# Performance work log

Measured on AMD Instinct MI355X. Metric: run time of the kernel, lower is better.

## Reference

```python
import jax, jax.numpy as jnp
import numpy as np

B, P, L1, D = 64, 16, 16, 1024  # images, people/img, object slots/img (slot0=no-object), feat dim
SP = 32   # flattened spatial (Conv_spatial output channels)
PROJ = 512
ACT = 29


def setup_inputs() -> dict:
    key = jax.random.key(0)
    ks = jax.random.split(key, 16)
    rn = lambda k, s, sc=1.0: jax.random.normal(k, s, dtype=jnp.float32) * sc
    w = 0.02  # weight init scale
    return {
        "people": rn(ks[0], (B, P, D)),
        "objects": rn(ks[1], (B, L1, D)),
        "context": rn(ks[2], (B, D)),
        "spatial": rn(ks[3], (B, P * L1, SP)),
        "Wvis_w": rn(ks[4], (3 * D, PROJ), w), "Wvis_b": jnp.zeros((PROJ,), jnp.float32),
        "Wspat_w": rn(ks[5], (SP, PROJ), w), "Wspat_b": jnp.zeros((PROJ,), jnp.float32),
        "Wip_w": rn(ks[6], (PROJ, 1), w), "Wip_b": jnp.zeros((1,), jnp.float32),
        "Wref_w": rn(ks[7], (PROJ, ACT), w), "Wref_b": jnp.zeros((ACT,), jnp.float32),
        "Watt_w": rn(ks[8], (PROJ, ACT), w), "Watt_b": jnp.zeros((ACT,), jnp.float32),
        "Woh_w": rn(ks[9], (D, D), w), "Woh_b": jnp.zeros((D,), jnp.float32),
        "Who_w": rn(ks[10], (D, D), w), "Who_b": jnp.zeros((D,), jnp.float32),
        "Wg_w": rn(ks[11], (2 * D, ACT), w), "Wg_b": jnp.zeros((ACT,), jnp.float32),
    }


def reference(people, objects, context, spatial,
              Wvis_w, Wvis_b, Wspat_w, Wspat_b, Wip_w, Wip_b,
              Wref_w, Wref_b, Watt_w, Watt_b,
              Woh_w, Woh_b, Who_w, Who_b, Wg_w, Wg_b):
    Bn, Pn, Dn = people.shape
    L = objects.shape[1]
    C = Bn * Pn * L

    # --- ROI.pairing: all (person, object-slot) pairs + image context -> [C, 3D]
    pe = jnp.broadcast_to(people[:, :, None, :], (Bn, Pn, L, Dn))
    ob = jnp.broadcast_to(objects[:, None, :, :], (Bn, Pn, L, Dn))
    cx = jnp.broadcast_to(context[:, None, None, :], (Bn, Pn, L, Dn))
    pairs = jnp.concatenate([pe, ob, cx], axis=-1).reshape(C, 3 * Dn)

    # --- attention / visual projection heads
    a_ho = jax.nn.relu(spatial.reshape(C, -1) @ Wspat_w + Wspat_b)   # W_Spat
    f_vis = jax.nn.relu(pairs @ Wvis_w + Wvis_b)                     # W_vis
    f_ref = f_vis * a_ho
    i_ho = f_ref @ Wip_w + Wip_b                                     # [C,1]
    interaction_prob = jax.nn.sigmoid(i_ho)
    p_ref = f_ref @ Wref_w + Wref_b                                  # [C,29]
    p_att = a_ho @ Watt_w + Watt_b                                   # [C,29]

    # --- graph message passing: adjacency = interaction probs, skipping slot 0 (no-object)
    adj = interaction_prob.reshape(Bn, Pn, L)[:, :, 1:]              # [B,P,O]
    oh = jax.nn.relu(objects[:, 1:] @ Woh_w + Woh_b)                 # W_oh on objects
    ho = jax.nn.relu(people @ Who_w + Who_b)                         # W_ho on people
    people_r = people + jnp.einsum('bpo,bod->bpd', adj, oh)
    objects_r = objects[:, 1:] + jnp.einsum('bpo,bpd->bod', adj, ho)
    objects_full = jnp.concatenate([objects[:, :1], objects_r], axis=1)  # re-attach no-object slot

    # --- refined all-pairs concat -> W_graph
    pe_r = jnp.broadcast_to(people_r[:, :, None, :], (Bn, Pn, L, Dn))
    ob_r = jnp.broadcast_to(objects_full[:, None, :, :], (Bn, Pn, L, Dn))
    pairs_g = jnp.concatenate([pe_r, ob_r], axis=-1).reshape(C, 2 * Dn)
    p_graph = pairs_g @ Wg_w + Wg_b                                  # [C,29]

    return (i_ho, p_ref, p_att, p_graph)
```

## Files before the change

### kernel.cpp

```cpp
#include <hip/hip_runtime.h>


typedef unsigned short u16;
typedef short s16x8 __attribute__((ext_vector_type(8)));
typedef float f32x4 __attribute__((ext_vector_type(4)));

__device__ __forceinline__ u16 f2b(float f) {
    union { float f; unsigned int i; } v; v.f = f;
    unsigned int r = (v.i + 0x7fffu + ((v.i >> 16) & 1u)) >> 16;
    return (u16)r;
}
__device__ __forceinline__ float b2f(u16 u) {
    union { float f; unsigned int i; } v; v.i = ((unsigned int)u) << 16; return v.f;
}
__device__ __forceinline__ unsigned int pack2(float x, float y) {
    return (unsigned int)f2b(x) | ((unsigned int)f2b(y) << 16);
}

#define OFF_WSPATT 0u
#define OFF_WREFT  32768u
#define OFF_WATTT  65536u
#define OFF_WGT    98304u
#define OFF_PP     229376u
#define OFF_PO     1277952u
#define OFF_PC     2326528u
#define OFF_ADJ    2392064u
#define OFF_HP     2457600u
#define OFF_HOF    2588672u
#define OFF_YH     2719744u
#define OFF_ZO     2850816u
#define ZERO_OFF   2457600u
#define ZERO_LEN   516096u
#define OFF_WVIST2 2973696u
#define OFF_WHOT2  6119424u
#define OFF_WOHT2  8216576u
#define OFF_PEOB   10313728u
#define OFF_OBJB   12410880u
#define OFF_CTXB   14508032u
#define OFF_SPATB  14639104u

__global__ __launch_bounds__(256) void prep_all(
    const float* __restrict__ people, const float* __restrict__ objects,
    const float* __restrict__ context, const float* __restrict__ spatial,
    const float* __restrict__ Wvis, const float* __restrict__ Who,
    const float* __restrict__ Woh, const float* __restrict__ Wspat,
    const float* __restrict__ Wref, const float* __restrict__ Watt,
    const float* __restrict__ Wg,
    u16* __restrict__ peoB, u16* __restrict__ objB, u16* __restrict__ ctxB,
    u16* __restrict__ spatB, u16* __restrict__ WvisT, u16* __restrict__ WhoT,
    u16* __restrict__ WohT, u16* __restrict__ WspatT, u16* __restrict__ WrefT,
    u16* __restrict__ WattT, u16* __restrict__ WgT)
{
    __shared__ float S[64][65];
    int bid = blockIdx.x, t = threadIdx.x;
    if (bid < 896) {
        const float* src; u16* dst; int N, K, kt, nt;
        int tb = bid;
        if (tb < 256)      { src = Who;  dst = WhoT;  K = 1024; N = 1024; kt = tb >> 4; nt = tb & 15; }
        else if (tb < 512) { tb -= 256; src = Woh;  dst = WohT;  K = 1024; N = 1024; kt = tb >> 4; nt = tb & 15; }
        else               { tb -= 512; src = Wvis; dst = WvisT; K = 3072; N = 512;  kt = tb >> 3; nt = tb & 7; }
        int k0 = kt * 64, n0 = nt * 64;
        int tx = t & 63, ty = t >> 6;
#pragma unroll
        for (int i = 0; i < 16; i++)
            S[ty + 4 * i][tx] = src[(size_t)(k0 + ty + 4 * i) * N + n0 + tx];
        __syncthreads();
#pragma unroll
        for (int i = 0; i < 16; i++)
            dst[(size_t)(n0 + ty + 4 * i) * K + k0 + tx] = f2b(S[tx][ty + 4 * i]);
        return;
    }
    int g = (bid - 896) * 256 + t;
    const int gsz = 512 * 256;
    for (int i = g; i < 524288; i += gsz) {
        float2 v = ((const float2*)people)[i];
        ((unsigned int*)peoB)[i] = pack2(v.x, v.y);
    }
    for (int i = g; i < 524288; i += gsz) {
        float2 v = ((const float2*)objects)[i];
        ((unsigned int*)objB)[i] = pack2(v.x, v.y);
    }
    for (int i = g; i < 32768; i += gsz) {
        float2 v = ((const float2*)context)[i];
        ((unsigned int*)ctxB)[i] = pack2(v.x, v.y);
    }
    for (int i = g; i < 262144; i += gsz) {
        float2 v = ((const float2*)spatial)[i];
        ((unsigned int*)spatB)[i] = pack2(v.x, v.y);
    }
    for (int i = g; i < 512 * 32; i += gsz) {
        int n = i >> 5, k = i & 31;
        WspatT[i] = f2b(Wspat[k * 512 + n]);
    }
    for (int i = g; i < 32 * 512; i += gsz) {
        int n = i >> 9, k = i & 511;
        WrefT[i] = (n < 29) ? f2b(Wref[k * 29 + n]) : (u16)0;
        WattT[i] = (n < 29) ? f2b(Watt[k * 29 + n]) : (u16)0;
    }
    for (int i = g; i < 32 * 2048; i += gsz) {
        int n = i >> 11, k = i & 2047;
        WgT[i] = (n < 29) ? f2b(Wg[k * 29 + n]) : (u16)0;
    }
}

__global__ __launch_bounds__(256) void fused_gemms(
    const u16* __restrict__ peoB, const u16* __restrict__ objB,
    const u16* __restrict__ ctxB, const u16* __restrict__ WvisT,
    const u16* __restrict__ WhoT, const float* __restrict__ Who_b,
    const u16* __restrict__ WohT, const float* __restrict__ Woh_b,
    const u16* __restrict__ WgT,
    u16* __restrict__ Pp, u16* __restrict__ Po, u16* __restrict__ Pc,
    float* __restrict__ Yh, float* __restrict__ Zo,
    float* __restrict__ Hp, float* __restrict__ HoF)
{
    __shared__ u16 T[64][72];
    int bid = blockIdx.x;
    int t = threadIdx.x;
    int lane = t & 63, w = t >> 6;
    int l16 = lane & 15, q = lane >> 4;
    int wy = w >> 1, wx = w & 1;

    if (bid < 264) {
        int bx = bid & 7, ty = bid >> 3;
        const u16* A; u16* outB; int koff, bm;
        if (ty < 16)      { A = peoB; outB = Pp; koff = 0;    bm = ty * 64; }
        else if (ty < 32) { A = objB; outB = Po; koff = 1024; bm = (ty - 16) * 64; }
        else              { A = ctxB; outB = Pc; koff = 2048; bm = 0; }
        int bn = bx * 64;

        const u16* ap0 = A + (size_t)(bm + wy * 32 + l16) * 1024 + q * 8;
        const u16* ap1 = ap0 + (size_t)16 * 1024;
        const u16* bp0 = WvisT + (size_t)(bn + wx * 32 + l16) * 3072 + koff + q * 8;
        const u16* bp1 = bp0 + (size_t)16 * 3072;

        f32x4 acc00 = {0,0,0,0}, acc01 = {0,0,0,0}, acc10 = {0,0,0,0}, acc11 = {0,0,0,0};
        s16x8 ca0 = *(const s16x8*)ap0,        ca1 = *(const s16x8*)ap1;
        s16x8 cb0 = *(const s16x8*)bp0,        cb1 = *(const s16x8*)bp1;
        s16x8 na0 = *(const s16x8*)(ap0 + 32), na1 = *(const s16x8*)(ap1 + 32);
        s16x8 nb0 = *(const s16x8*)(bp0 + 32), nb1 = *(const s16x8*)(bp1 + 32);
        ap0 += 64; ap1 += 64; bp0 += 64; bp1 += 64;
        for (int it = 0; it < 30; it++) {
            s16x8 ta0 = *(const s16x8*)ap0, ta1 = *(const s16x8*)ap1;
            s16x8 tb0 = *(const s16x8*)bp0, tb1 = *(const s16x8*)bp1;
            ap0 += 32; ap1 += 32; bp0 += 32; bp1 += 32;
            acc00 = __builtin_amdgcn_mfma_f32_16x16x32_bf16(ca0, cb0, acc00, 0, 0, 0);
            acc01 = __builtin_amdgcn_mfma_f32_16x16x32_bf16(ca0, cb1, acc01, 0, 0, 0);
            acc10 = __builtin_amdgcn_mfma_f32_16x16x32_bf16(ca1, cb0, acc10, 0, 0, 0);
            acc11 = __builtin_amdgcn_mfma_f32_16x16x32_bf16(ca1, cb1, acc11, 0, 0, 0);
            ca0 = na0; ca1 = na1; cb0 = nb0; cb1 = nb1;
            na0 = ta0; na1 = ta1; nb0 = tb0; nb1 = tb1;
        }
        acc00 = __builtin_amdgcn_mfma_f32_16x16x32_bf16(ca0, cb0, acc00, 0, 0, 0);
        acc01 = __builtin_amdgcn_mfma_f32_16x16x32_bf16(ca0, cb1, acc01, 0, 0, 0);
        acc10 = __builtin_amdgcn_mfma_f32_16x16x32_bf16(ca1, cb0, acc10, 0, 0, 0);
        acc11 = __builtin_amdgcn_mfma_f32_16x16x32_bf16(ca1, cb1, acc11, 0, 0, 0);
        acc00 = __builtin_amdgcn_mfma_f32_16x16x32_bf16(na0, nb0, acc00, 0, 0, 0);
        acc01 = __builtin_amdgcn_mfma_f32_16x16x32_bf16(na0, nb1, acc01, 0, 0, 0);
        acc10 = __builtin_amdgcn_mfma_f32_16x16x32_bf16(na1, nb0, acc10, 0, 0, 0);
        acc11 = __builtin_amdgcn_mfma_f32_16x16x32_bf16(na1, nb1, acc11, 0, 0, 0);

        f32x4 accs[2][2] = {{acc00, acc01}, {acc10, acc11}};
#pragma unroll
        for (int ii = 0; ii < 2; ii++)
#pragma unroll
            for (int jj = 0; jj < 2; jj++) {
                int col = bn + wx * 32 + jj * 16 + l16;
#pragma unroll
                for (int r = 0; r < 4; r++) {
                    int row = bm + wy * 32 + ii * 16 + q * 4 + r;
                    outB[(size_t)row * 512 + col] = f2b(accs[ii][jj][r]);
                }
            }
    } else if (bid < 760) {
        int r3 = bid - 264;
        int z, rt, nbt;
        if (r3 < 256) { z = 0; rt = r3 >> 4; nbt = r3 & 15; }
        else          { z = 1; r3 -= 256; rt = r3 >> 4; nbt = r3 & 15; }
        const u16* A    = z ? objB : peoB;
        const u16* W1T  = z ? WohT : WhoT;
        const float* bb = z ? Woh_b : Who_b;
        const u16* Wg2  = z ? WgT : WgT + 1024;
        float* U        = z ? Zo : Yh;
        int m0 = rt * 64, nb = nbt * 64;

        int r0 = m0 + wy * 32 + l16;
        int r1 = r0 + 16;
        if (z) { r0 = (r0 / 15) * 16 + (r0 % 15) + 1;
                 r1 = (r1 / 15) * 16 + (r1 % 15) + 1; }
        const u16* ap0 = A + (size_t)r0 * 1024 + q * 8;
        const u16* ap1 = A + (size_t)r1 * 1024 + q * 8;
        const u16* bp0 = W1T + (size_t)(nb + wx * 32 + l16) * 1024 + q * 8;
        const u16* bp1 = bp0 + (size_t)16 * 1024;

        f32x4 acc00 = {0,0,0,0}, acc01 = {0,0,0,0}, acc10 = {0,0,0,0}, acc11 = {0,0,0,0};
        s16x8 ca0 = *(const s16x8*)ap0,        ca1 = *(const s16x8*)ap1;
        s16x8 cb0 = *(const s16x8*)bp0,        cb1 = *(const s16x8*)bp1;
        s16x8 na0 = *(const s16x8*)(ap0 + 32), na1 = *(const s16x8*)(ap1 + 32);
        s16x8 nb0 = *(const s16x8*)(bp0 + 32), nb1 = *(const s16x8*)(bp1 + 32);
        ap0 += 64; ap1 += 64; bp0 += 64; bp1 += 64;
        for (int it = 0; it < 30; it++) {
            s16x8 ta0 = *(const s16x8*)ap0, ta1 = *(const s16x8*)ap1;
            s16x8 tb0 = *(const s16x8*)bp0, tb1 = *(const s16x8*)bp1;
            ap0 += 32; ap1 += 32; bp0 += 32; bp1 += 32;
            acc00 = __builtin_amdgcn_mfma_f32_16x16x32_bf16(ca0, cb0, acc00, 0, 0, 0);
            acc01 = __builtin_amdgcn_mfma_f32_16x16x32_bf16(ca0, cb1, acc01, 0, 0, 0);
            acc10 = __builtin_amdgcn_mfma_f32_16x16x32_bf16(ca1, cb0, acc10, 0, 0, 0);
            acc11 = __builtin_amdgcn_mfma_f32_16x16x32_bf16(ca1, cb1, acc11, 0, 0, 0);
            ca0 = na0; ca1 = na1; cb0 = nb0; cb1 = nb1;
            na0 = ta0; na1 = ta1; nb0 = tb0; nb1 = tb1;
        }
        acc00 = __builtin_amdgcn_mfma_f32_16x16x32_bf16(ca0, cb0, acc00, 0, 0, 0);
        acc01 = __builtin_amdgcn_mfma_f32_16x16x32_bf16(ca0, cb1, acc01, 0, 0, 0);
        acc10 = __builtin_amdgcn_mfma_f32_16x16x32_bf16(ca1, cb0, acc10, 0, 0, 0);
        acc11 = __builtin_amdgcn_mfma_f32_16x16x32_bf16(ca1, cb1, acc11, 0, 0, 0);
        acc00 = __builtin_amdgcn_mfma_f32_16x16x32_bf16(na0, nb0, acc00, 0, 0, 0);
        acc01 = __builtin_amdgcn_mfma_f32_16x16x32_bf16(na0, nb1, acc01, 0, 0, 0);
        acc10 = __builtin_amdgcn_mfma_f32_16x16x32_bf16(na1, nb0, acc10, 0, 0, 0);
        acc11 = __builtin_amdgcn_mfma_f32_16x16x32_bf16(na1, nb1, acc11, 0, 0, 0);

        f32x4 accs[2][2] = {{acc00, acc01}, {acc10, acc11}};
#pragma unroll
        for (int ii = 0; ii < 2; ii++)
#pragma unroll
            for (int jj = 0; jj < 2; jj++) {
                int col = wx * 32 + jj * 16 + l16;
                float bv = bb[nb + col];
#pragma unroll
                for (int rr = 0; rr < 4; rr++) {
                    float v = accs[ii][jj][rr] + bv;
                    T[wy * 32 + ii * 16 + q * 4 + rr][col] = f2b(fmaxf(v, 0.f));
                }
            }
        __syncthreads();

        f32x4 s20 = {0,0,0,0}, s21 = {0,0,0,0};
#pragma unroll
        for (int kk = 0; kk < 64; kk += 32) {
            s16x8 a2 = *(const s16x8*)(&T[w * 16 + l16][kk + q * 8]);
            s16x8 b20 = *(const s16x8*)(Wg2 + (size_t)l16 * 2048 + nb + kk + q * 8);
            s16x8 b21 = *(const s16x8*)(Wg2 + (size_t)(16 + l16) * 2048 + nb + kk + q * 8);
            s20 = __builtin_amdgcn_mfma_f32_16x16x32_bf16(a2, b20, s20, 0, 0, 0);
            s21 = __builtin_amdgcn_mfma_f32_16x16x32_bf16(a2, b21, s21, 0, 0, 0);
        }
#pragma unroll
        for (int rr = 0; rr < 4; rr++) {
            int row = m0 + w * 16 + q * 4 + rr;
            atomicAdd(&U[(size_t)row * 32 + l16], s20[rr]);
            atomicAdd(&U[(size_t)row * 32 + 16 + l16], s21[rr]);
        }
    } else {
        int r3 = bid - 760;
        int bx = r3 & 7, by = (r3 >> 3) & 7, z = r3 >> 6;
        const u16* A  = z ? objB : peoB;
        const u16* BT = z ? WgT + 1024 : WgT;
        float* outF   = z ? HoF : Hp;
        int bm = bx * 128 + w * 32;
        int kb = by * 128;
        const u16* ap0 = A + (size_t)(bm + l16) * 1024 + kb + q * 8;
        const u16* ap1 = A + (size_t)(bm + 16 + l16) * 1024 + kb + q * 8;
        const u16* bp0 = BT + (size_t)l16 * 2048 + kb + q * 8;
        const u16* bp1 = BT + (size_t)(16 + l16) * 2048 + kb + q * 8;
        f32x4 acc00 = {0,0,0,0}, acc01 = {0,0,0,0}, acc10 = {0,0,0,0}, acc11 = {0,0,0,0};
        s16x8 ca0 = *(const s16x8*)ap0,        ca1 = *(const s16x8*)ap1;
        s16x8 cb0 = *(const s16x8*)bp0,        cb1 = *(const s16x8*)bp1;
        s16x8 na0 = *(const s16x8*)(ap0 + 32), na1 = *(const s16x8*)(ap1 + 32);
        s16x8 nb0 = *(const s16x8*)(bp0 + 32), nb1 = *(const s16x8*)(bp1 + 32);
        ap0 += 64; ap1 += 64; bp0 += 64; bp1 += 64;
#pragma unroll
        for (int it = 0; it < 2; it++) {
            s16x8 ta0 = *(const s16x8*)ap0, ta1 = *(const s16x8*)ap1;
            s16x8 tb0 = *(const s16x8*)bp0, tb1 = *(const s16x8*)bp1;
            ap0 += 32; ap1 += 32; bp0 += 32; bp1 += 32;
            acc00 = __builtin_amdgcn_mfma_f32_16x16x32_bf16(ca0, cb0, acc00, 0, 0, 0);
            acc01 = __builtin_amdgcn_mfma_f32_16x16x32_bf16(ca0, cb1, acc01, 0, 0, 0);
            acc10 = __builtin_amdgcn_mfma_f32_16x16x32_bf16(ca1, cb0, acc10, 0, 0, 0);
            acc11 = __builtin_amdgcn_mfma_f32_16x16x32_bf16(ca1, cb1, acc11, 0, 0, 0);
            ca0 = na0; ca1 = na1; cb0 = nb0; cb1 = nb1;
            na0 = ta0; na1 = ta1; nb0 = tb0; nb1 = tb1;
        }
        acc00 = __builtin_amdgcn_mfma_f32_16x16x32_bf16(ca0, cb0, acc00, 0, 0, 0);
        acc01 = __builtin_amdgcn_mfma_f32_16x16x32_bf16(ca0, cb1, acc01, 0, 0, 0);
        acc10 = __builtin_amdgcn_mfma_f32_16x16x32_bf16(ca1, cb0, acc10, 0, 0, 0);
        acc11 = __builtin_amdgcn_mfma_f32_16x16x32_bf16(ca1, cb1, acc11, 0, 0, 0);
        acc00 = __builtin_amdgcn_mfma_f32_16x16x32_bf16(na0, nb0, acc00, 0, 0, 0);
        acc01 = __builtin_amdgcn_mfma_f32_16x16x32_bf16(na0, nb1, acc01, 0, 0, 0);
        acc10 = __builtin_amdgcn_mfma_f32_16x16x32_bf16(na1, nb0, acc10, 0, 0, 0);
        acc11 = __builtin_amdgcn_mfma_f32_16x16x32_bf16(na1, nb1, acc11, 0, 0, 0);
        f32x4 accs[2][2] = {{acc00, acc01}, {acc10, acc11}};
#pragma unroll
        for (int ii = 0; ii < 2; ii++)
#pragma unroll
            for (int jj = 0; jj < 2; jj++)
#pragma unroll
                for (int r = 0; r < 4; r++)
                    atomicAdd(&outF[(size_t)(bm + ii * 16 + q * 4 + r) * 32 + jj * 16 + l16],
                              accs[ii][jj][r]);
    }
}

__global__ __launch_bounds__(256) void mega(
    const u16* __restrict__ spatB, const u16* __restrict__ WspatT,
    const float* __restrict__ bspat,
    const u16* __restrict__ Pp, const u16* __restrict__ Po,
    const u16* __restrict__ Pc, const float* __restrict__ bvis,
    const u16* __restrict__ WrefT, const float* __restrict__ bref,
    const u16* __restrict__ WattT, const float* __restrict__ batt,
    const float* __restrict__ wip, const float* __restrict__ bip,
    float* __restrict__ outI, float* __restrict__ outRef,
    float* __restrict__ outAtt, float* __restrict__ adjw)
{
    __shared__ u16 tile[32][512];
    __shared__ float part[32][8];
    __shared__ float wipS[512];
    int t = threadIdx.x;
    int c0 = blockIdx.x * 32;
    int lane = t & 63, w = t >> 6;
    int l16 = lane & 15, q = lane >> 4;

    {
        float2 u = *(const float2*)(wip + t * 2);
        wipS[t * 2]     = u.x;
        wipS[t * 2 + 1] = u.y;
    }

    {
        s16x8 a0 = *(const s16x8*)(spatB + (size_t)(c0 + l16) * 32 + q * 8);
        s16x8 a1 = *(const s16x8*)(spatB + (size_t)(c0 + 16 + l16) * 32 + q * 8);
        const u16* wb = WspatT + (size_t)(w * 128 + l16) * 32 + q * 8;
        s16x8 cb = *(const s16x8*)wb;
        s16x8 nb_ = *(const s16x8*)(wb + 16 * 32);
        wb += 32 * 32;
#pragma unroll
        for (int nt = 0; nt < 8; nt++) {
            s16x8 tb;
            if (nt < 6) { tb = *(const s16x8*)wb; wb += 16 * 32; }
            int n = w * 128 + nt * 16;
            f32x4 acc0 = {0,0,0,0}, acc1 = {0,0,0,0};
            acc0 = __builtin_amdgcn_mfma_f32_16x16x32_bf16(a0, cb, acc0, 0, 0, 0);
            acc1 = __builtin_amdgcn_mfma_f32_16x16x32_bf16(a1, cb, acc1, 0, 0, 0);
            cb = nb_; nb_ = tb;
            float bias = bspat[n + l16];
#pragma unroll
            for (int r = 0; r < 4; r++) {
                tile[q * 4 + r][n + l16]      = f2b(fmaxf(acc0[r] + bias, 0.f));
                tile[16 + q * 4 + r][n + l16] = f2b(fmaxf(acc1[r] + bias, 0.f));
            }
        }
    }
    __syncthreads();

    {
        int rt = w >> 1, ct = w & 1;
        const u16* bp = WattT + (size_t)(ct * 16 + l16) * 512 + q * 8;
        f32x4 acc = {0,0,0,0};
        s16x8 cb = *(const s16x8*)bp;
        s16x8 nb_ = *(const s16x8*)(bp + 32);
        bp += 64;
        for (int i = 0; i < 14; i++) {
            s16x8 tb = *(const s16x8*)bp; bp += 32;
            s16x8 a = *(const s16x8*)(&tile[rt * 16 + l16][i * 32 + q * 8]);
            acc = __builtin_amdgcn_mfma_f32_16x16x32_bf16(a, cb, acc, 0, 0, 0);
            cb = nb_; nb_ = tb;
        }
        {
            s16x8 a = *(const s16x8*)(&tile[rt * 16 + l16][14 * 32 + q * 8]);
            acc = __builtin_amdgcn_mfma_f32_16x16x32_bf16(a, cb, acc, 0, 0, 0);
            a = *(const s16x8*)(&tile[rt * 16 + l16][15 * 32 + q * 8]);
            acc = __builtin_amdgcn_mfma_f32_16x16x32_bf16(a, nb_, acc, 0, 0, 0);
        }
        int col = ct * 16 + l16;
        if (col < 29) {
            float bias = batt[col];
#pragma unroll
            for (int r = 0; r < 4; r++) {
                int row = c0 + rt * 16 + q * 4 + r;
                outAtt[(size_t)row * 29 + col] = acc[r] + bias;
            }
        }
    }
    __syncthreads();

    {
        int row = t >> 3, g = t & 7;
        int c = c0 + row;
        int rp = c >> 4, bimg = c >> 8;
        int ro = bimg * 16 + (c & 15);
        const u16* ppr = Pp + (size_t)rp * 512;
        const u16* por = Po + (size_t)ro * 512;
        const u16* pcr = Pc + (size_t)bimg * 512;
        float ps = 0.f;
#pragma unroll 4
        for (int j = 0; j < 64; j += 2) {
            int col = g * 64 + j;
            unsigned int upp = *(const unsigned int*)(ppr + col);
            unsigned int upo = *(const unsigned int*)(por + col);
            unsigned int upc = *(const unsigned int*)(pcr + col);
            float2 bv = *(const float2*)(bvis + col);
            unsigned int uah = *(const unsigned int*)(&tile[row][col]);
            float fv0 = fmaxf(b2f((u16)(upp & 0xffff)) + b2f((u16)(upo & 0xffff))
                            + b2f((u16)(upc & 0xffff)) + bv.x, 0.f);
            float fv1 = fmaxf(b2f((u16)(upp >> 16)) + b2f((u16)(upo >> 16))
                            + b2f((u16)(upc >> 16)) + bv.y, 0.f);
            float fr0 = fv0 * b2f((u16)(uah & 0xffff));
            float fr1 = fv1 * b2f((u16)(uah >> 16));
            *(unsigned int*)(&tile[row][col]) = pack2(fr0, fr1);
            ps += fr0 * wipS[col] + fr1 * wipS[col + 1];
        }
        part[row][g] = ps;
    }
    __syncthreads();

    if (t < 32) {
        float s = part[t][0] + part[t][1] + part[t][2] + part[t][3]
                + part[t][4] + part[t][5] + part[t][6] + part[t][7] + bip[0];
        outI[c0 + t] = s;
        adjw[c0 + t] = 1.f / (1.f + expf(-s));
    }

    {
        int rt = w >> 1, ct = w & 1;
        const u16* bp = WrefT + (size_t)(ct * 16 + l16) * 512 + q * 8;
        f32x4 acc = {0,0,0,0};
        s16x8 cb = *(const s16x8*)bp;
        s16x8 nb_ = *(const s16x8*)(bp + 32);
        bp += 64;
        for (int i = 0; i < 14; i++) {
            s16x8 tb = *(const s16x8*)bp; bp += 32;
            s16x8 a = *(const s16x8*)(&tile[rt * 16 + l16][i * 32 + q * 8]);
            acc = __builtin_amdgcn_mfma_f32_16x16x32_bf16(a, cb, acc, 0, 0, 0);
            cb = nb_; nb_ = tb;
        }
        {
            s16x8 a = *(const s16x8*)(&tile[rt * 16 + l16][14 * 32 + q * 8]);
            acc = __builtin_amdgcn_mfma_f32_16x16x32_bf16(a, cb, acc, 0, 0, 0);
            a = *(const s16x8*)(&tile[rt * 16 + l16][15 * 32 + q * 8]);
            acc = __builtin_amdgcn_mfma_f32_16x16x32_bf16(a, nb_, acc, 0, 0, 0);
        }
        int col = ct * 16 + l16;
        if (col < 29) {
            float bias = bref[col];
#pragma unroll
            for (int r = 0; r < 4; r++) {
                int row = c0 + rt * 16 + q * 4 + r;
                outRef[(size_t)row * 29 + col] = acc[r] + bias;
            }
        }
    }
}

__global__ __launch_bounds__(256) void pgraph2(
    const float* __restrict__ adjw, const float* __restrict__ Hp,
    const float* __restrict__ HoF, const float* __restrict__ Yh,
    const float* __restrict__ Zo, const float* __restrict__ bg,
    float* __restrict__ outG)
{
    int b = blockIdx.x, t = threadIdx.x;
    __shared__ float adjS[16][16];
    __shared__ float YhS[16][32];
    __shared__ float ZoS[15][32];
    __shared__ float PA[16][32];
    __shared__ float OA[16][32];
    adjS[t >> 4][t & 15] = adjw[b * 256 + t];
    for (int i = t; i < 512; i += 256)
        YhS[i >> 5][i & 31] = Yh[(size_t)(b * 16 + (i >> 5)) * 32 + (i & 31)];
    for (int i = t; i < 480; i += 256)
        ZoS[i >> 5][i & 31] = Zo[(size_t)(b * 15 + (i >> 5)) * 32 + (i & 31)];
    __syncthreads();
    for (int i = t; i < 512; i += 256) {
        int p = i >> 5, j = i & 31;
        float s = 0.f;
#pragma unroll
        for (int o = 0; o < 15; o++) s += adjS[p][o + 1] * ZoS[o][j];
        PA[p][j] = s;
        float s2 = 0.f;
#pragma unroll
        for (int pp = 0; pp < 16; pp++) s2 += adjS[pp][p] * YhS[pp][j];
        OA[p][j] = s2;
    }
    __syncthreads();
    int p = t >> 4, l = t & 15;
    const float* hp = Hp + (size_t)(b * 16 + p) * 32;
    const float* ho = HoF + (size_t)(b * 16 + l) * 32;
    size_t c = (size_t)b * 256 + t;
    for (int j = 0; j < 29; j++) {
        float v = hp[j] + ho[j] + bg[j] + PA[p][j];
        if (l >= 1) v += OA[l][j];
        outG[c * 29 + j] = v;
    }
}

extern "C" void kernel_launch(void* const* d_in, const int* in_sizes, int n_in,
                              void* d_out, int out_size, void* d_ws, size_t ws_size,
                              hipStream_t stream)
{
    const float* people  = (const float*)d_in[0];
    const float* objects = (const float*)d_in[1];
    const float* context = (const float*)d_in[2];
    const float* spatial = (const float*)d_in[3];
    const float* Wvis_w  = (const float*)d_in[4];
    const float* Wvis_b  = (const float*)d_in[5];
    const float* Wspat_w = (const float*)d_in[6];
    const float* Wspat_b = (const float*)d_in[7];
    const float* Wip_w   = (const float*)d_in[8];
    const float* Wip_b   = (const float*)d_in[9];
    const float* Wref_w  = (const float*)d_in[10];
    const float* Wref_b  = (const float*)d_in[11];
    const float* Watt_w  = (const float*)d_in[12];
    const float* Watt_b  = (const float*)d_in[13];
    const float* Woh_w   = (const float*)d_in[14];
    const float* Woh_b   = (const float*)d_in[15];
    const float* Who_w   = (const float*)d_in[16];
    const float* Who_b   = (const float*)d_in[17];
    const float* Wg_w    = (const float*)d_in[18];
    const float* Wg_b    = (const float*)d_in[19];

    char* ws = (char*)d_ws;
    u16* WspatT = (u16*)(ws + OFF_WSPATT);
    u16* WrefT  = (u16*)(ws + OFF_WREFT);
    u16* WattT  = (u16*)(ws + OFF_WATTT);
    u16* WgT    = (u16*)(ws + OFF_WGT);
    u16* Ppb    = (u16*)(ws + OFF_PP);
    u16* Pob    = (u16*)(ws + OFF_PO);
    u16* Pcb    = (u16*)(ws + OFF_PC);
    float* adjw = (float*)(ws + OFF_ADJ);
    float* Hp   = (float*)(ws + OFF_HP);
    float* HoF  = (float*)(ws + OFF_HOF);
    float* Yh   = (float*)(ws + OFF_YH);
    float* Zo   = (float*)(ws + OFF_ZO);
    u16* WvisT2 = (u16*)(ws + OFF_WVIST2);
    u16* WhoT2  = (u16*)(ws + OFF_WHOT2);
    u16* WohT2  = (u16*)(ws + OFF_WOHT2);
    u16* peoB   = (u16*)(ws + OFF_PEOB);
    u16* objB   = (u16*)(ws + OFF_OBJB);
    u16* ctxB   = (u16*)(ws + OFF_CTXB);
    u16* spatB  = (u16*)(ws + OFF_SPATB);

    float* outI   = (float*)d_out;
    float* outRef = outI + 16384;
    float* outAtt = outI + 491520;
    float* outG   = outI + 966656;

    hipMemsetAsync(ws + ZERO_OFF, 0, ZERO_LEN, stream);

    prep_all<<<1408, 256, 0, stream>>>(people, objects, context, spatial,
        Wvis_w, Who_w, Woh_w, Wspat_w, Wref_w, Watt_w, Wg_w,
        peoB, objB, ctxB, spatB, WvisT2, WhoT2, WohT2,
        WspatT, WrefT, WattT, WgT);

    fused_gemms<<<888, 256, 0, stream>>>(peoB, objB, ctxB, WvisT2,
        WhoT2, Who_b, WohT2, Woh_b, WgT,
        Ppb, Pob, Pcb, Yh, Zo, Hp, HoF);

    mega<<<512, 256, 0, stream>>>(spatB, WspatT, Wspat_b,
                                  Ppb, Pob, Pcb, Wvis_b,
                                  WrefT, Wref_b, WattT, Watt_b,
                                  Wip_w, Wip_b,
                                  outI, outRef, outAtt, adjw);

    pgraph2<<<64, 256, 0, stream>>>(adjw, Hp, HoF, Yh, Zo, Wg_b, outG);
}
```

Measured before the change: 188.8 us.

## Split-K the Wvis projection GEMM and co-schedule mega with graph GEMMs

The Wvis partial-projection GEMM moves into its own kernel with a split-K of 2, accumulating into fp32 buffers via atomics instead of bf16 stores. The Who/Woh and Wg GEMM blocks leave that kernel and join the pair-head (mega) work in one combined launch, so independent GEMMs overlap with the per-pair head computation. This adds a second memset of about 4 MB, fp32 atomic traffic, and reads fp32 projections instead of bf16 in the head stage.

New measurement: 204.6 us. 1.08x slower.

```diff
diff --git a/kernel.cpp b/kernel.cpp
--- a/kernel.cpp
+++ b/kernel.cpp
@@ -21,9 +21,6 @@
 #define OFF_WREFT  32768u
 #define OFF_WATTT  65536u
 #define OFF_WGT    98304u
-#define OFF_PP     229376u
-#define OFF_PO     1277952u
-#define OFF_PC     2326528u
 #define OFF_ADJ    2392064u
 #define OFF_HP     2457600u
 #define OFF_HOF    2588672u
@@ -38,6 +35,11 @@
 #define OFF_OBJB   12410880u
 #define OFF_CTXB   14508032u
 #define OFF_SPATB  14639104u
+#define OFF_PPF    15687680u
+#define OFF_POF    17784832u
+#define OFF_PCF    19881984u
+#define ZERO2_OFF  15687680u
+#define ZERO2_LEN  4325376u
 
 __global__ __launch_bounds__(256) void prep_all(
     const float* __restrict__ people, const float* __restrict__ objects,
@@ -103,35 +105,240 @@
     }
 }
 
-__global__ __launch_bounds__(256) void fused_gemms(
+__global__ __launch_bounds__(256) void gemm3s(
     const u16* __restrict__ peoB, const u16* __restrict__ objB,
     const u16* __restrict__ ctxB, const u16* __restrict__ WvisT,
+    float* __restrict__ PpF, float* __restrict__ PoF, float* __restrict__ PcF)
+{
+    int t = threadIdx.x;
+    int lane = t & 63, w = t >> 6;
+    int l16 = lane & 15, q = lane >> 4;
+    int wy = w >> 1, wx = w & 1;
+    int ty = blockIdx.y;
+    const u16* A; float* outF; int koff, bm;
+    if (ty < 16)      { A = peoB; outF = PpF; koff = 0;    bm = ty * 64; }
+    else if (ty < 32) { A = objB; outF = PoF; koff = 1024; bm = (ty - 16) * 64; }
+    else              { A = ctxB; outF = PcF; bm = 0; koff = 2048; }
+    int bn = blockIdx.x * 64;
+    int k0 = blockIdx.z * 512;
+
+    const u16* ap0 = A + (size_t)(bm + wy * 32 + l16) * 1024 + k0 + q * 8;
+    const u16* ap1 = ap0 + (size_t)16 * 1024;
+    const u16* bp0 = WvisT + (size_t)(bn + wx * 32 + l16) * 3072 + koff + k0 + q * 8;
+    const u16* bp1 = bp0 + (size_t)16 * 3072;
+
+    f32x4 acc00 = {0,0,0,0}, acc01 = {0,0,0,0}, acc10 = {0,0,0,0}, acc11 = {0,0,0,0};
+    s16x8 ca0 = *(const s16x8*)ap0,        ca1 = *(const s16x8*)ap1;
+    s16x8 cb0 = *(const s16x8*)bp0,        cb1 = *(const s16x8*)bp1;
+    s16x8 na0 = *(const s16x8*)(ap0 + 32), na1 = *(const s16x8*)(ap1 + 32);
+    s16x8 nb0 = *(const s16x8*)(bp0 + 32), nb1 = *(const s16x8*)(bp1 + 32);
+    ap0 += 64; ap1 += 64; bp0 += 64; bp1 += 64;
+    for (int it = 0; it < 14; it++) {
+        s16x8 ta0 = *(const s16x8*)ap0, ta1 = *(const s16x8*)ap1;
+        s16x8 tb0 = *(const s16x8*)bp0, tb1 = *(const s16x8*)bp1;
+        ap0 += 32; ap1 += 32; bp0 += 32; bp1 += 32;
+        acc00 = __builtin_amdgcn_mfma_f32_16x16x32_bf16(ca0, cb0, acc00, 0, 0, 0);
+        acc01 = __builtin_amdgcn_mfma_f32_16x16x32_bf16(ca0, cb1, acc01, 0, 0, 0);
+        acc10 = __builtin_amdgcn_mfma_f32_16x16x32_bf16(ca1, cb0, acc10, 0, 0, 0);
+        acc11 = __builtin_amdgcn_mfma_f32_16x16x32_bf16(ca1, cb1, acc11, 0, 0, 0);
+        ca0 = na0; ca1 = na1; cb0 = nb0; cb1 = nb1;
+        na0 = ta0; na1 = ta1; nb0 = tb0; nb1 = tb1;
+    }
+    acc00 = __builtin_amdgcn_mfma_f32_16x16x32_bf16(ca0, cb0, acc00, 0, 0, 0);
+    acc01 = __builtin_amdgcn_mfma_f32_16x16x32_bf16(ca0, cb1, acc01, 0, 0, 0);
+    acc10 = __builtin_amdgcn_mfma_f32_16x16x32_bf16(ca1, cb0, acc10, 0, 0, 0);
+    acc11 = __builtin_amdgcn_mfma_f32_16x16x32_bf16(ca1, cb1, acc11, 0, 0, 0);
+    acc00 = __builtin_amdgcn_mfma_f32_16x16x32_bf16(na0, nb0, acc00, 0, 0, 0);
+    acc01 = __builtin_amdgcn_mfma_f32_16x16x32_bf16(na0, nb1, acc01, 0, 0, 0);
+    acc10 = __builtin_amdgcn_mfma_f32_16x16x32_bf16(na1, nb0, acc10, 0, 0, 0);
+    acc11 = __builtin_amdgcn_mfma_f32_16x16x32_bf16(na1, nb1, acc11, 0, 0, 0);
+
+    f32x4 accs[2][2] = {{acc00, acc01}, {acc10, acc11}};
+#pragma unroll
+    for (int ii = 0; ii < 2; ii++)
+#pragma unroll
+        for (int jj = 0; jj < 2; jj++) {
+            int col = bn + wx * 32 + jj * 16 + l16;
+#pragma unroll
+            for (int r = 0; r < 4; r++) {
+                int row = bm + wy * 32 + ii * 16 + q * 4 + r;
+                atomicAdd(&outF[(size_t)row * 512 + col], accs[ii][jj][r]);
+            }
+        }
+}
+
+__global__ __launch_bounds__(256) void combo(
+    const u16* __restrict__ spatB, const u16* __restrict__ WspatT,
+    const float* __restrict__ bspat,
+    const float* __restrict__ PpF, const float* __restrict__ PoF,
+    const float* __restrict__ PcF, const float* __restrict__ bvis,
+    const u16* __restrict__ WrefT, const float* __restrict__ bref,
+    const u16* __restrict__ WattT, const float* __restrict__ batt,
+    const float* __restrict__ wip, const float* __restrict__ bip,
+    float* __restrict__ outI, float* __restrict__ outRef,
+    float* __restrict__ outAtt, float* __restrict__ adjw,
+    const u16* __restrict__ peoB, const u16* __restrict__ objB,
     const u16* __restrict__ WhoT, const float* __restrict__ Who_b,
     const u16* __restrict__ WohT, const float* __restrict__ Woh_b,
     const u16* __restrict__ WgT,
-    u16* __restrict__ Pp, u16* __restrict__ Po, u16* __restrict__ Pc,
     float* __restrict__ Yh, float* __restrict__ Zo,
     float* __restrict__ Hp, float* __restrict__ HoF)
 {
-    __shared__ u16 T[64][72];
+    __shared__ __align__(16) char smem[35840];
     int bid = blockIdx.x;
     int t = threadIdx.x;
     int lane = t & 63, w = t >> 6;
     int l16 = lane & 15, q = lane >> 4;
     int wy = w >> 1, wx = w & 1;
 
-    if (bid < 264) {
-        int bx = bid & 7, ty = bid >> 3;
-        const u16* A; u16* outB; int koff, bm;
-        if (ty < 16)      { A = peoB; outB = Pp; koff = 0;    bm = ty * 64; }
-        else if (ty < 32) { A = objB; outB = Po; koff = 1024; bm = (ty - 16) * 64; }
-        else              { A = ctxB; outB = Pc; koff = 2048; bm = 0; }
-        int bn = bx * 64;
-
-        const u16* ap0 = A + (size_t)(bm + wy * 32 + l16) * 1024 + q * 8;
-        const u16* ap1 = ap0 + (size_t)16 * 1024;
-        const u16* bp0 = WvisT + (size_t)(bn + wx * 32 + l16) * 3072 + koff + q * 8;
-        const u16* bp1 = bp0 + (size_t)16 * 3072;
+    if (bid < 512) {
+        u16 (*tile)[512] = (u16(*)[512])smem;
+        float (*part)[8] = (float(*)[8])(smem + 32768);
+        float* wipS = (float*)(smem + 33792);
+        int c0 = bid * 32;
+        {
+            float2 u = *(const float2*)(wip + t * 2);
+            wipS[t * 2]     = u.x;
+            wipS[t * 2 + 1] = u.y;
+        }
+        {
+            s16x8 a0 = *(const s16x8*)(spatB + (size_t)(c0 + l16) * 32 + q * 8);
+            s16x8 a1 = *(const s16x8*)(spatB + (size_t)(c0 + 16 + l16) * 32 + q * 8);
+            const u16* wb = WspatT + (size_t)(w * 128 + l16) * 32 + q * 8;
+            s16x8 cb = *(const s16x8*)wb;
+            s16x8 nb_ = *(const s16x8*)(wb + 16 * 32);
+            wb += 32 * 32;
+#pragma unroll
+            for (int nt = 0; nt < 8; nt++) {
+                s16x8 tb = nb_;
+                if (nt < 6) { tb = *(const s16x8*)wb; wb += 16 * 32; }
+                int n = w * 128 + nt * 16;
+                f32x4 acc0 = {0,0,0,0}, acc1 = {0,0,0,0};
+                acc0 = __builtin_amdgcn_mfma_f32_16x16x32_bf16(a0, cb, acc0, 0, 0, 0);
+                acc1 = __builtin_amdgcn_mfma_f32_16x16x32_bf16(a1, cb, acc1, 0, 0, 0);
+                cb = nb_; nb_ = tb;
+                float bias = bspat[n + l16];
+#pragma unroll
+                for (int r = 0; r < 4; r++) {
+                    tile[q * 4 + r][n + l16]      = f2b(fmaxf(acc0[r] + bias, 0.f));
+                    tile[16 + q * 4 + r][n + l16] = f2b(fmaxf(acc1[r] + bias, 0.f));
+                }
+            }
+        }
+        __syncthreads();
+        {
+            int rt = w >> 1, ct = w & 1;
+            const u16* bp = WattT + (size_t)(ct * 16 + l16) * 512 + q * 8;
+            f32x4 acc = {0,0,0,0};
+            s16x8 cb = *(const s16x8*)bp;
+            s16x8 nb_ = *(const s16x8*)(bp + 32);
+            bp += 64;
+            for (int i = 0; i < 14; i++) {
+                s16x8 tb = *(const s16x8*)bp; bp += 32;
+                s16x8 a = *(const s16x8*)(&tile[rt * 16 + l16][i * 32 + q * 8]);
+                acc = __builtin_amdgcn_mfma_f32_16x16x32_bf16(a, cb, acc, 0, 0, 0);
+                cb = nb_; nb_ = tb;
+            }
+            {
+                s16x8 a = *(const s16x8*)(&tile[rt * 16 + l16][14 * 32 + q * 8]);
+                acc = __builtin_amdgcn_mfma_f32_16x16x32_bf16(a, cb, acc, 0, 0, 0);
+                a = *(const s16x8*)(&tile[rt * 16 + l16][15 * 32 + q * 8]);
+                acc = __builtin_amdgcn_mfma_f32_16x16x32_bf16(a, nb_, acc, 0, 0, 0);
+            }
+            int col = ct * 16 + l16;
+            if (col < 29) {
+                float bias = batt[col];
+#pragma unroll
+                for (int r = 0; r < 4; r++) {
+                    int row = c0 + rt * 16 + q * 4 + r;
+                    outAtt[(size_t)row * 29 + col] = acc[r] + bias;
+                }
+            }
+        }
+        __syncthreads();
+        {
+            int row = t >> 3, g = t & 7;
+            int c = c0 + row;
+            int rp = c >> 4, bimg = c >> 8;
+            int ro = bimg * 16 + (c & 15);
+            const float* ppr = PpF + (size_t)rp * 512;
+            const float* por = PoF + (size_t)ro * 512;
+            const float* pcr = PcF + (size_t)bimg * 512;
+            float ps = 0.f;
+#pragma unroll 4
+            for (int j = 0; j < 64; j += 2) {
+                int col = g * 64 + j;
+                float2 pp = *(const float2*)(ppr + col);
+                float2 po = *(const float2*)(por + col);
+                float2 pc = *(const float2*)(pcr + col);
+                float2 bv = *(const float2*)(bvis + col);
+                unsigned int uah = *(const unsigned int*)(&tile[row][col]);
+                float fv0 = fmaxf(pp.x + po.x + pc.x + bv.x, 0.f);
+                float fv1 = fmaxf(pp.y + po.y + pc.y + bv.y, 0.f);
+                float fr0 = fv0 * b2f((u16)(uah & 0xffff));
+                float fr1 = fv1 * b2f((u16)(uah >> 16));
+                *(unsigned int*)(&tile[row][col]) = pack2(fr0, fr1);
+                ps += fr0 * wipS[col] + fr1 * wipS[col + 1];
+            }
+            part[row][g] = ps;
+        }
+        __syncthreads();
+        if (t < 32) {
+            float s = part[t][0] + part[t][1] + part[t][2] + part[t][3]
+                    + part[t][4] + part[t][5] + part[t][6] + part[t][7] + bip[0];
+            outI[c0 + t] = s;
+            adjw[c0 + t] = 1.f / (1.f + expf(-s));
+        }
+        {
+            int rt = w >> 1, ct = w & 1;
+            const u16* bp = WrefT + (size_t)(ct * 16 + l16) * 512 + q * 8;
+            f32x4 acc = {0,0,0,0};
+            s16x8 cb = *(const s16x8*)bp;
+            s16x8 nb_ = *(const s16x8*)(bp + 32);
+            bp += 64;
+            for (int i = 0; i < 14; i++) {
+                s16x8 tb = *(const s16x8*)bp; bp += 32;
+                s16x8 a = *(const s16x8*)(&tile[rt * 16 + l16][i * 32 + q * 8]);
+                acc = __builtin_amdgcn_mfma_f32_16x16x32_bf16(a, cb, acc, 0, 0, 0);
+                cb = nb_; nb_ = tb;
+            }
+            {
+                s16x8 a = *(const s16x8*)(&tile[rt * 16 + l16][14 * 32 + q * 8]);
+                acc = __builtin_amdgcn_mfma_f32_16x16x32_bf16(a, cb, acc, 0, 0, 0);
+                a = *(const s16x8*)(&tile[rt * 16 + l16][15 * 32 + q * 8]);
+                acc = __builtin_amdgcn_mfma_f32_16x16x32_bf16(a, nb_, acc, 0, 0, 0);
+            }
+            int col = ct * 16 + l16;
+            if (col < 29) {
+                float bias = bref[col];
+#pragma unroll
+                for (int r = 0; r < 4; r++) {
+                    int row = c0 + rt * 16 + q * 4 + r;
+                    outRef[(size_t)row * 29 + col] = acc[r] + bias;
+                }
+            }
+        }
+    } else if (bid < 1008) {
+        u16 (*T)[72] = (u16(*)[72])smem;
+        int r3 = bid - 512;
+        int z, rt, nbt;
+        if (r3 < 256) { z = 0; rt = r3 >> 4; nbt = r3 & 15; }
+        else          { z = 1; r3 -= 256; rt = r3 >> 4; nbt = r3 & 15; }
+        const u16* A    = z ? objB : peoB;
+        const u16* W1T  = z ? WohT : WhoT;
+        const float* bb = z ? Woh_b : Who_b;
+        const u16* Wg2  = z ? WgT : WgT + 1024;
+        float* U        = z ? Zo : Yh;
+        int m0 = rt * 64, nb = nbt * 64;
+
+        int r0 = m0 + wy * 32 + l16;
+        int r1 = r0 + 16;
+        if (z) { r0 = (r0 / 15) * 16 + (r0 % 15) + 1;
+                 r1 = (r1 / 15) * 16 + (r1 % 15) + 1; }
+        const u16* ap0 = A + (size_t)r0 * 1024 + q * 8;
+        const u16* ap1 = A + (size_t)r1 * 1024 + q * 8;
+        const u16* bp0 = W1T + (size_t)(nb + wx * 32 + l16) * 1024 + q * 8;
+        const u16* bp1 = bp0 + (size_t)16 * 1024;
 
         f32x4 acc00 = {0,0,0,0}, acc01 = {0,0,0,0}, acc10 = {0,0,0,0}, acc11 = {0,0,0,0};
         s16x8 ca0 = *(const s16x8*)ap0,        ca1 = *(const s16x8*)ap1;
@@ -164,65 +371,6 @@
         for (int ii = 0; ii < 2; ii++)
 #pragma unroll
             for (int jj = 0; jj < 2; jj++) {
-                int col = bn + wx * 32 + jj * 16 + l16;
-#pragma unroll
-                for (int r = 0; r < 4; r++) {
-                    int row = bm + wy * 32 + ii * 16 + q * 4 + r;
-                    outB[(size_t)row * 512 + col] = f2b(accs[ii][jj][r]);
-                }
-            }
-    } else if (bid < 760) {
-        int r3 = bid - 264;
-        int z, rt, nbt;
-        if (r3 < 256) { z = 0; rt = r3 >> 4; nbt = r3 & 15; }
-        else          { z = 1; r3 -= 256; rt = r3 >> 4; nbt = r3 & 15; }
-        const u16* A    = z ? objB : peoB;
-        const u16* W1T  = z ? WohT : WhoT;
-        const float* bb = z ? Woh_b : Who_b;
-        const u16* Wg2  = z ? WgT : WgT + 1024;
-        float* U        = z ? Zo : Yh;
-        int m0 = rt * 64, nb = nbt * 64;
-
-        int r0 = m0 + wy * 32 + l16;
-        int r1 = r0 + 16;
-        if (z) { r0 = (r0 / 15) * 16 + (r0 % 15) + 1;
-                 r1 = (r1 / 15) * 16 + (r1 % 15) + 1; }
-        const u16* ap0 = A + (size_t)r0 * 1024 + q * 8;
-        const u16* ap1 = A + (size_t)r1 * 1024 + q * 8;
-        const u16* bp0 = W1T + (size_t)(nb + wx * 32 + l16) * 1024 + q * 8;
-        const u16* bp1 = bp0 + (size_t)16 * 1024;
-
-        f32x4 acc00 = {0,0,0,0}, acc01 = {0,0,0,0}, acc10 = {0,0,0,0}, acc11 = {0,0,0,0};
-        s16x8 ca0 = *(const s16x8*)ap0,        ca1 = *(const s16x8*)ap1;
-        s16x8 cb0 = *(const s16x8*)bp0,        cb1 = *(const s16x8*)bp1;
-        s16x8 na0 = *(const s16x8*)(ap0 + 32), na1 = *(const s16x8*)(ap1 + 32);
-        s16x8 nb0 = *(const s16x8*)(bp0 + 32), nb1 = *(const s16x8*)(bp1 + 32);
-        ap0 += 64; ap1 += 64; bp0 += 64; bp1 += 64;
-        for (int it = 0; it < 30; it++) {
-            s16x8 ta0 = *(const s16x8*)ap0, ta1 = *(const s16x8*)ap1;
-            s16x8 tb0 = *(const s16x8*)bp0, tb1 = *(const s16x8*)bp1;
-            ap0 += 32; ap1 += 32; bp0 += 32; bp1 += 32;
-            acc00 = __builtin_amdgcn_mfma_f32_16x16x32_bf16(ca0, cb0, acc00, 0, 0, 0);
-            acc01 = __builtin_amdgcn_mfma_f32_16x16x32_bf16(ca0, cb1, acc01, 0, 0, 0);
-            acc10 = __builtin_amdgcn_mfma_f32_16x16x32_bf16(ca1, cb0, acc10, 0, 0, 0);
-            acc11 = __builtin_amdgcn_mfma_f32_16x16x32_bf16(ca1, cb1, acc11, 0, 0, 0);
-            ca0 = na0; ca1 = na1; cb0 = nb0; cb1 = nb1;
-            na0 = ta0; na1 = ta1; nb0 = tb0; nb1 = tb1;
-        }
-        acc00 = __builtin_amdgcn_mfma_f32_16x16x32_bf16(ca0, cb0, acc00, 0, 0, 0);
-        acc01 = __builtin_amdgcn_mfma_f32_16x16x32_bf16(ca0, cb1, acc01, 0, 0, 0);
-        acc10 = __builtin_amdgcn_mfma_f32_16x16x32_bf16(ca1, cb0, acc10, 0, 0, 0);
-        acc11 = __builtin_amdgcn_mfma_f32_16x16x32_bf16(ca1, cb1, acc11, 0, 0, 0);
-        acc00 = __builtin_amdgcn_mfma_f32_16x16x32_bf16(na0, nb0, acc00, 0, 0, 0);
-        acc01 = __builtin_amdgcn_mfma_f32_16x16x32_bf16(na0, nb1, acc01, 0, 0, 0);
-        acc10 = __builtin_amdgcn_mfma_f32_16x16x32_bf16(na1, nb0, acc10, 0, 0, 0);
-        acc11 = __builtin_amdgcn_mfma_f32_16x16x32_bf16(na1, nb1, acc11, 0, 0, 0);
-
-        f32x4 accs[2][2] = {{acc00, acc01}, {acc10, acc11}};
-#pragma unroll
-        for (int ii = 0; ii < 2; ii++)
-#pragma unroll
-            for (int jj = 0; jj < 2; jj++) {
                 int col = wx * 32 + jj * 16 + l16;
                 float bv = bb[nb + col];
 #pragma unroll
@@ -249,7 +397,7 @@
             atomicAdd(&U[(size_t)row * 32 + 16 + l16], s21[rr]);
         }
     } else {
-        int r3 = bid - 760;
+        int r3 = bid - 1008;
         int bx = r3 & 7, by = (r3 >> 3) & 7, z = r3 >> 6;
         const u16* A  = z ? objB : peoB;
         const u16* BT = z ? WgT + 1024 : WgT;
@@ -295,156 +443,6 @@
                 for (int r = 0; r < 4; r++)
                     atomicAdd(&outF[(size_t)(bm + ii * 16 + q * 4 + r) * 32 + jj * 16 + l16],
                               accs[ii][jj][r]);
-    }
-}
-
-__global__ __launch_bounds__(256) void mega(
-    const u16* __restrict__ spatB, const u16* __restrict__ WspatT,
-    const float* __restrict__ bspat,
-    const u16* __restrict__ Pp, const u16* __restrict__ Po,
-    const u16* __restrict__ Pc, const float* __restrict__ bvis,
-    const u16* __restrict__ WrefT, const float* __restrict__ bref,
-    const u16* __restrict__ WattT, const float* __restrict__ batt,
-    const float* __restrict__ wip, const float* __restrict__ bip,
-    float* __restrict__ outI, float* __restrict__ outRef,
-    float* __restrict__ outAtt, float* __restrict__ adjw)
-{
-    __shared__ u16 tile[32][512];
-    __shared__ float part[32][8];
-    __shared__ float wipS[512];
-    int t = threadIdx.x;
-    int c0 = blockIdx.x * 32;
-    int lane = t & 63, w = t >> 6;
-    int l16 = lane & 15, q = lane >> 4;
-
-    {
-        float2 u = *(const float2*)(wip + t * 2);
-        wipS[t * 2]     = u.x;
-        wipS[t * 2 + 1] = u.y;
-    }
-
-    {
-        s16x8 a0 = *(const s16x8*)(spatB + (size_t)(c0 + l16) * 32 + q * 8);
-        s16x8 a1 = *(const s16x8*)(spatB + (size_t)(c0 + 16 + l16) * 32 + q * 8);
-        const u16* wb = WspatT + (size_t)(w * 128 + l16) * 32 + q * 8;
-        s16x8 cb = *(const s16x8*)wb;
-        s16x8 nb_ = *(const s16x8*)(wb + 16 * 32);
-        wb += 32 * 32;
-#pragma unroll
-        for (int nt = 0; nt < 8; nt++) {
-            s16x8 tb;
-            if (nt < 6) { tb = *(const s16x8*)wb; wb += 16 * 32; }
-            int n = w * 128 + nt * 16;
-            f32x4 acc0 = {0,0,0,0}, acc1 = {0,0,0,0};
-            acc0 = __builtin_amdgcn_mfma_f32_16x16x32_bf16(a0, cb, acc0, 0, 0, 0);
-            acc1 = __builtin_amdgcn_mfma_f32_16x16x32_bf16(a1, cb, acc1, 0, 0, 0);
-            cb = nb_; nb_ = tb;
-            float bias = bspat[n + l16];
-#pragma unroll
-            for (int r = 0; r < 4; r++) {
-                tile[q * 4 + r][n + l16]      = f2b(fmaxf(acc0[r] + bias, 0.f));
-                tile[16 + q * 4 + r][n + l16] = f2b(fmaxf(acc1[r] + bias, 0.f));
-            }
-        }
-    }
-    __syncthreads();
-
-    {
-        int rt = w >> 1, ct = w & 1;
-        const u16* bp = WattT + (size_t)(ct * 16 + l16) * 512 + q * 8;
-        f32x4 acc = {0,0,0,0};
-        s16x8 cb = *(const s16x8*)bp;
-        s16x8 nb_ = *(const s16x8*)(bp + 32);
-        bp += 64;
-        for (int i = 0; i < 14; i++) {
-            s16x8 tb = *(const s16x8*)bp; bp += 32;
-            s16x8 a = *(const s16x8*)(&tile[rt * 16 + l16][i * 32 + q * 8]);
-            acc = __builtin_amdgcn_mfma_f32_16x16x32_bf16(a, cb, acc, 0, 0, 0);
-            cb = nb_; nb_ = tb;
-        }
-        {
-            s16x8 a = *(const s16x8*)(&tile[rt * 16 + l16][14 * 32 + q * 8]);
-            acc = __builtin_amdgcn_mfma_f32_16x16x32_bf16(a, cb, acc, 0, 0, 0);
-            a = *(const s16x8*)(&tile[rt * 16 + l16][15 * 32 + q * 8]);
-            acc = __builtin_amdgcn_mfma_f32_16x16x32_bf16(a, nb_, acc, 0, 0, 0);
-        }
-        int col = ct * 16 + l16;
-        if (col < 29) {
-            float bias = batt[col];
-#pragma unroll
-            for (int r = 0; r < 4; r++) {
-                int row = c0 + rt * 16 + q * 4 + r;
-                outAtt[(size_t)row * 29 + col] = acc[r] + bias;
-            }
-        }
-    }
-    __syncthreads();
-
-    {
-        int row = t >> 3, g = t & 7;
-        int c = c0 + row;
-        int rp = c >> 4, bimg = c >> 8;
-        int ro = bimg * 16 + (c & 15);
-        const u16* ppr = Pp + (size_t)rp * 512;
-        const u16* por = Po + (size_t)ro * 512;
-        const u16* pcr = Pc + (size_t)bimg * 512;
-        float ps = 0.f;
-#pragma unroll 4
-        for (int j = 0; j < 64; j += 2) {
-            int col = g * 64 + j;
-            unsigned int upp = *(const unsigned int*)(ppr + col);
-            unsigned int upo = *(const unsigned int*)(por + col);
-            unsigned int upc = *(const unsigned int*)(pcr + col);
-            float2 bv = *(const float2*)(bvis + col);
-            unsigned int uah = *(const unsigned int*)(&tile[row][col]);
-            float fv0 = fmaxf(b2f((u16)(upp & 0xffff)) + b2f((u16)(upo & 0xffff))
-                            + b2f((u16)(upc & 0xffff)) + bv.x, 0.f);
-            float fv1 = fmaxf(b2f((u16)(upp >> 16)) + b2f((u16)(upo >> 16))
-                            + b2f((u16)(upc >> 16)) + bv.y, 0.f);
-            float fr0 = fv0 * b2f((u16)(uah & 0xffff));
-            float fr1 = fv1 * b2f((u16)(uah >> 16));
-            *(unsigned int*)(&tile[row][col]) = pack2(fr0, fr1);
-            ps += fr0 * wipS[col] + fr1 * wipS[col + 1];
-        }
-        part[row][g] = ps;
-    }
-    __syncthreads();
-
-    if (t < 32) {
-        float s = part[t][0] + part[t][1] + part[t][2] + part[t][3]
-                + part[t][4] + part[t][5] + part[t][6] + part[t][7] + bip[0];
-        outI[c0 + t] = s;
-        adjw[c0 + t] = 1.f / (1.f + expf(-s));
-    }
-
-    {
-        int rt = w >> 1, ct = w & 1;
-        const u16* bp = WrefT + (size_t)(ct * 16 + l16) * 512 + q * 8;
-        f32x4 acc = {0,0,0,0};
-        s16x8 cb = *(const s16x8*)bp;
-        s16x8 nb_ = *(const s16x8*)(bp + 32);
-        bp += 64;
-        for (int i = 0; i < 14; i++) {
-            s16x8 tb = *(const s16x8*)bp; bp += 32;
-            s16x8 a = *(const s16x8*)(&tile[rt * 16 + l16][i * 32 + q * 8]);
-            acc = __builtin_amdgcn_mfma_f32_16x16x32_bf16(a, cb, acc, 0, 0, 0);
-            cb = nb_; nb_ = tb;
-        }
-        {
-            s16x8 a = *(const s16x8*)(&tile[rt * 16 + l16][14 * 32 + q * 8]);
-            acc = __builtin_amdgcn_mfma_f32_16x16x32_bf16(a, cb, acc, 0, 0, 0);
-            a = *(const s16x8*)(&tile[rt * 16 + l16][15 * 32 + q * 8]);
-            acc = __builtin_amdgcn_mfma_f32_16x16x32_bf16(a, nb_, acc, 0, 0, 0);
-        }
-        int col = ct * 16 + l16;
-        if (col < 29) {
-            float bias = bref[col];
-#pragma unroll
-            for (int r = 0; r < 4; r++) {
-                int row = c0 + rt * 16 + q * 4 + r;
-                outRef[(size_t)row * 29 + col] = acc[r] + bias;
-            }
-        }
     }
 }
 
@@ -519,9 +517,6 @@
     u16* WrefT  = (u16*)(ws + OFF_WREFT);
     u16* WattT  = (u16*)(ws + OFF_WATTT);
     u16* WgT    = (u16*)(ws + OFF_WGT);
-    u16* Ppb    = (u16*)(ws + OFF_PP);
-    u16* Pob    = (u16*)(ws + OFF_PO);
-    u16* Pcb    = (u16*)(ws + OFF_PC);
     float* adjw = (float*)(ws + OFF_ADJ);
     float* Hp   = (float*)(ws + OFF_HP);
     float* HoF  = (float*)(ws + OFF_HOF);
@@ -534,6 +529,9 @@
     u16* objB   = (u16*)(ws + OFF_OBJB);
     u16* ctxB   = (u16*)(ws + OFF_CTXB);
     u16* spatB  = (u16*)(ws + OFF_SPATB);
+    float* PpF  = (float*)(ws + OFF_PPF);
+    float* PoF  = (float*)(ws + OFF_POF);
+    float* PcF  = (float*)(ws + OFF_PCF);
 
     float* outI   = (float*)d_out;
     float* outRef = outI + 16384;
@@ -541,21 +539,21 @@
     float* outG   = outI + 966656;
 
     hipMemsetAsync(ws + ZERO_OFF, 0, ZERO_LEN, stream);
+    hipMemsetAsync(ws + ZERO2_OFF, 0, ZERO2_LEN, stream);
 
     prep_all<<<1408, 256, 0, stream>>>(people, objects, context, spatial,
         Wvis_w, Who_w, Woh_w, Wspat_w, Wref_w, Watt_w, Wg_w,
         peoB, objB, ctxB, spatB, WvisT2, WhoT2, WohT2,
         WspatT, WrefT, WattT, WgT);
 
-    fused_gemms<<<888, 256, 0, stream>>>(peoB, objB, ctxB, WvisT2,
-        WhoT2, Who_b, WohT2, Woh_b, WgT,
-        Ppb, Pob, Pcb, Yh, Zo, Hp, HoF);
-
-    mega<<<512, 256, 0, stream>>>(spatB, WspatT, Wspat_b,
-                                  Ppb, Pob, Pcb, Wvis_b,
-                                  WrefT, Wref_b, WattT, Watt_b,
-                                  Wip_w, Wip_b,
-                                  outI, outRef, outAtt, adjw);
+    gemm3s<<<dim3(8, 33, 2), 256, 0, stream>>>(peoB, objB, ctxB, WvisT2,
+                                               PpF, PoF, PcF);
+
+    combo<<<1136, 256, 0, stream>>>(spatB, WspatT, Wspat_b,
+        PpF, PoF, PcF, Wvis_b, WrefT, Wref_b, WattT, Watt_b,
+        Wip_w, Wip_b, outI, outRef, outAtt, adjw,
+        peoB, objB, WhoT2, Who_b, WohT2, Woh_b, WgT,
+        Yh, Zo, Hp, HoF);
 
     pgraph2<<<64, 256, 0, stream>>>(adjw, Hp, HoF, Yh, Zo, Wg_b, outG);
 }
```
